# Optimization experiments

Hardware: AMD Instinct MI355X
Metric: run time of the kernel (lower is better)

The kernel has to match this reference:

```python
import jax, jax.numpy as jnp
import numpy as np

B, N, D = 4, 16384, 128       # batch, tokens (mesh points), input_dim
H, DH = 8, 64                 # heads, dim_head
INNER = H * DH


def setup_inputs() -> dict:
    key = jax.random.key(0)
    ks = jax.random.split(key, 7)
    s = 0.02  # weight init scale
    return {
        "queries": jax.random.normal(ks[0], (B, N, D), jnp.float32),
        "keys":    jax.random.normal(ks[1], (B, N, D), jnp.float32),
        "values":  jax.random.normal(ks[2], (B, N, D), jnp.float32),
        "Wq": jax.random.normal(ks[3], (INNER, D), jnp.float32) * s,
        "Wk": jax.random.normal(ks[4], (INNER, D), jnp.float32) * s,
        "Wo": jax.random.normal(ks[5], (D, INNER), jnp.float32) * s,
        "bo": jnp.zeros((D,), jnp.float32),
    }


def _split_heads(x, b, n):
    # [b, n, h*d] -> [b, h, n, d]
    return x.reshape(b, n, H, DH).transpose(0, 2, 1, 3)


def reference(queries, keys, values, Wq, Wk, Wo, bo):
    b, n, _ = queries.shape
    q = _split_heads(queries @ Wq.T, b, n)
    k = _split_heads(keys    @ Wk.T, b, n)
    # NOTE: original source applies to_k to values (bug kept for faithfulness)
    v = _split_heads(values  @ Wk.T, b, n)
    # Galerkin linear attention, associative order: q @ (k^T v) / n.
    # (In the runnable no-mask path the instance norms are computed but
    #  discarded by the original code, so they are omitted here.)
    dots = jnp.einsum('bhnd,bhne->bhde', k, v)          # [b,h,d,d]
    out = jnp.einsum('bhnd,bhde->bhne', q, dots) / n    # [b,h,n,d]
    out = out.transpose(0, 2, 1, 3).reshape(b, n, INNER)
    return out @ Wo.T + bo
```

## Files before the change

kernel.cpp:

```cpp
#include <hip/hip_runtime.h>
#include <hip/hip_bf16.h>

#define BB    4
#define NN    16384
#define DD    128
#define HH    8
#define DHH   64
#define INNER 512
#define PC    64

typedef __attribute__((ext_vector_type(8))) short bf16x8;
typedef __attribute__((ext_vector_type(4))) short short4_t;
typedef __attribute__((ext_vector_type(4))) float f32x4;
typedef unsigned short ushort_t;

#define MFMA(a, b, c) __builtin_amdgcn_mfma_f32_16x16x32_bf16((a), (b), (c), 0, 0, 0)

__device__ __forceinline__ short f2bf(float x) {
    union { float f; unsigned u; } v; v.f = x;
    unsigned u = v.u;
    u += 0x7fffu + ((u >> 16) & 1u);
    return (short)(u >> 16);
}

__device__ __forceinline__ float bf2f(ushort_t us) {
    union { unsigned u; float f; } v;
    v.u = ((unsigned)us) << 16;
    return v.f;
}

__device__ __forceinline__ bf16x8 load_row8(const float* __restrict__ p) {
    f32x4 a = *(const f32x4*)p;
    f32x4 b = *(const f32x4*)(p + 4);
    bf16x8 r;
    r[0] = f2bf(a[0]); r[1] = f2bf(a[1]); r[2] = f2bf(a[2]); r[3] = f2bf(a[3]);
    r[4] = f2bf(b[0]); r[5] = f2bf(b[1]); r[6] = f2bf(b[2]); r[7] = f2bf(b[3]);
    return r;
}

__device__ __forceinline__ bf16x8 load_col8(const float* __restrict__ p, int stride) {
    bf16x8 r;
#pragma unroll
    for (int j = 0; j < 8; ++j) r[j] = f2bf(p[(size_t)j * stride]);
    return r;
}

__global__ __launch_bounds__(512) void k1_partialS_ab(
        const float* __restrict__ keys, const float* __restrict__ vals,
        const float* __restrict__ Wq, const float* __restrict__ Wk,
        const float* __restrict__ Wo,
        ushort_t* __restrict__ partial, ushort_t* __restrict__ Abf,
        ushort_t* __restrict__ BTbf) {
    const int lane = threadIdx.x & 63;
    const int w    = threadIdx.x >> 6;
    const int ml   = lane & 15;
    const int quad = lane >> 4;

    __shared__ short tK[2][32][132];
    __shared__ short tV[2][32][132];

    if (blockIdx.x < BB * PC) {
        const int b     = blockIdx.x >> 6;
        const int chunk = blockIdx.x & (PC - 1);
        const int r0    = chunk * (NN / PC);
        const int mw    = w & 3;
        const int nw    = w >> 2;

        const float* kbase = keys + (size_t)b * NN * DD;
        const float* vbase = vals + (size_t)b * NN * DD;

        const int lin0 = (int)threadIdx.x;
        const int ca0  = (2 * mw + 0) * 16 + ml;
        const int ca1  = (2 * mw + 1) * 16 + ml;

        f32x4 acc[2][4];
#pragma unroll
        for (int i = 0; i < 2; ++i)
#pragma unroll
            for (int t = 0; t < 4; ++t) acc[i][t] = (f32x4){0.f, 0.f, 0.f, 0.f};

        {
            const float* kp = kbase + (size_t)r0 * DD;
            const float* vp = vbase + (size_t)r0 * DD;
#pragma unroll
            for (int it = 0; it < 2; ++it) {
                const int lin = lin0 + it * 512;
                const int row = lin >> 5;
                const int c4  = (lin & 31) << 2;
                f32x4 kk = *(const f32x4*)(kp + (size_t)row * DD + c4);
                f32x4 vv = *(const f32x4*)(vp + (size_t)row * DD + c4);
                short4_t ks, vs;
#pragma unroll
                for (int j = 0; j < 4; ++j) { ks[j] = f2bf(kk[j]); vs[j] = f2bf(vv[j]); }
                *(short4_t*)&tK[0][row][c4] = ks;
                *(short4_t*)&tV[0][row][c4] = vs;
            }
        }
        __syncthreads();

        for (int s = 0; s < 8; ++s) {
            const int cur  = s & 1;
            const bool more = (s < 7);

            f32x4 kreg[2], vreg[2];
            if (more) {
                const float* kp = kbase + (size_t)(r0 + (s + 1) * 32) * DD;
                const float* vp = vbase + (size_t)(r0 + (s + 1) * 32) * DD;
#pragma unroll
                for (int it = 0; it < 2; ++it) {
                    const int lin = lin0 + it * 512;
                    const int row = lin >> 5;
                    const int c4  = (lin & 31) << 2;
                    kreg[it] = *(const f32x4*)(kp + (size_t)row * DD + c4);
                    vreg[it] = *(const f32x4*)(vp + (size_t)row * DD + c4);
                }
            }

            {
                bf16x8 a0, a1;
#pragma unroll
                for (int j = 0; j < 8; ++j) {
                    a0[j] = tK[cur][quad * 8 + j][ca0];
                    a1[j] = tK[cur][quad * 8 + j][ca1];
                }
#pragma unroll
                for (int t = 0; t < 4; ++t) {
                    const int cb = (nw * 4 + t) * 16 + ml;
                    bf16x8 bf;
#pragma unroll
                    for (int j = 0; j < 8; ++j) bf[j] = tV[cur][quad * 8 + j][cb];
                    acc[0][t] = MFMA(a0, bf, acc[0][t]);
                    acc[1][t] = MFMA(a1, bf, acc[1][t]);
                }
            }

            if (more) {
                __syncthreads();
                const int nb = cur ^ 1;
#pragma unroll
                for (int it = 0; it < 2; ++it) {
                    const int lin = lin0 + it * 512;
                    const int row = lin >> 5;
                    const int c4  = (lin & 31) << 2;
                    short4_t ks, vs;
#pragma unroll
                    for (int j = 0; j < 4; ++j) {
                        ks[j] = f2bf(kreg[it][j]);
                        vs[j] = f2bf(vreg[it][j]);
                    }
                    *(short4_t*)&tK[nb][row][c4] = ks;
                    *(short4_t*)&tV[nb][row][c4] = vs;
                }
                __syncthreads();
            }
        }

        ushort_t* outp = partial + (size_t)blockIdx.x * DD * DD;
#pragma unroll
        for (int i = 0; i < 2; ++i) {
            const int mrow = (2 * mw + i) * 16 + quad * 4;
#pragma unroll
            for (int t = 0; t < 4; ++t) {
                const int col = (nw * 4 + t) * 16 + ml;
#pragma unroll
                for (int r = 0; r < 4; ++r)
                    outp[(size_t)(mrow + r) * DD + col] = (ushort_t)f2bf(acc[i][t][r]);
            }
        }
    } else {
        const int ab    = blockIdx.x - BB * PC;
        const int h     = ab & 7;
        const int which = ab >> 3;
        const float* Wkh = Wk + (size_t)h * DHH * DD;

        f32x4 acc[8];
#pragma unroll
        for (int t = 0; t < 8; ++t) acc[t] = (f32x4){0.f, 0.f, 0.f, 0.f};

        if (which == 0) {
            const float* Wqh = Wq + (size_t)h * DHH * DD;
#pragma unroll
            for (int kc = 0; kc < 2; ++kc) {
                const int d0 = kc * 32 + quad * 8;
                bf16x8 a = load_col8(Wqh + (size_t)d0 * DD + w * 16 + ml, DD);
#pragma unroll
                for (int t = 0; t < 8; ++t) {
                    bf16x8 bf = load_col8(Wkh + (size_t)d0 * DD + t * 16 + ml, DD);
                    acc[t] = MFMA(a, bf, acc[t]);
                }
            }
            ushort_t* dst = Abf + (size_t)h * DD * DD;
#pragma unroll
            for (int t = 0; t < 8; ++t)
#pragma unroll
                for (int r = 0; r < 4; ++r)
                    dst[(size_t)(w * 16 + quad * 4 + r) * DD + t * 16 + ml] =
                        (ushort_t)f2bf(acc[t][r]);
        } else {
#pragma unroll
            for (int kc = 0; kc < 2; ++kc) {
                const int e0 = kc * 32 + quad * 8;
                bf16x8 a = load_row8(Wo + (size_t)(w * 16 + ml) * INNER + h * DHH + e0);
#pragma unroll
                for (int t = 0; t < 8; ++t) {
                    bf16x8 bf = load_col8(Wkh + (size_t)e0 * DD + t * 16 + ml, DD);
                    acc[t] = MFMA(a, bf, acc[t]);
                }
            }
            ushort_t* dst = BTbf + (size_t)h * DD * DD;
#pragma unroll
            for (int t = 0; t < 8; ++t)
#pragma unroll
                for (int r = 0; r < 4; ++r)
                    dst[(size_t)(w * 16 + quad * 4 + r) * DD + t * 16 + ml] =
                        (ushort_t)f2bf(acc[t][r]);
        }
    }
}

__global__ __launch_bounds__(256) void k2_reduce(
        const ushort_t* __restrict__ partial, float* __restrict__ S,
        float* __restrict__ G) {
    const int t   = blockIdx.x * 256 + threadIdx.x;
    const int b   = t >> 14;
    const int idx = t & 16383;
    const ushort_t* p = partial + ((size_t)b * PC) * DD * DD + idx;
    float s = 0.f;
#pragma unroll 16
    for (int c = 0; c < PC; ++c) s += bf2f(p[(size_t)c * DD * DD]);
    S[t] = s;
    G[t] = 0.f;
}

__global__ __launch_bounds__(256) void k3_middle(
        const float* __restrict__ S, const ushort_t* __restrict__ Abf,
        const ushort_t* __restrict__ BTbf, float* __restrict__ G) {
    const int b    = blockIdx.x >> 3;
    const int h    = blockIdx.x & 7;
    const int lane = threadIdx.x & 63;
    const int w    = threadIdx.x >> 6;
    const int ml   = lane & 15;
    const int quad = lane >> 4;

    __shared__ short T[128 * 136];

    const float*    Sb = S    + (size_t)b * DD * DD;
    const ushort_t* Ah = Abf  + (size_t)h * DD * DD;
    const ushort_t* Bh = BTbf + (size_t)h * DD * DD;

    {
        f32x4 acc[2][8];
#pragma unroll
        for (int i = 0; i < 2; ++i)
#pragma unroll
            for (int t = 0; t < 8; ++t) acc[i][t] = (f32x4){0.f, 0.f, 0.f, 0.f};
#pragma unroll
        for (int kc = 0; kc < 4; ++kc) {
            const int c0 = kc * 32 + quad * 8;
            bf16x8 a[2];
#pragma unroll
            for (int i = 0; i < 2; ++i)
                a[i] = *(const bf16x8*)&Ah[(size_t)((2 * w + i) * 16 + ml) * DD + c0];
#pragma unroll
            for (int t = 0; t < 8; ++t) {
                bf16x8 bf = load_col8(Sb + (size_t)c0 * DD + t * 16 + ml, DD);
                acc[0][t] = MFMA(a[0], bf, acc[0][t]);
                acc[1][t] = MFMA(a[1], bf, acc[1][t]);
            }
        }
#pragma unroll
        for (int i = 0; i < 2; ++i)
#pragma unroll
            for (int t = 0; t < 8; ++t)
#pragma unroll
                for (int r = 0; r < 4; ++r)
                    T[((2 * w + i) * 16 + quad * 4 + r) * 136 + t * 16 + ml] =
                        f2bf(acc[i][t][r]);
    }
    __syncthreads();

    {
        f32x4 acc[2][8];
#pragma unroll
        for (int i = 0; i < 2; ++i)
#pragma unroll
            for (int t = 0; t < 8; ++t) acc[i][t] = (f32x4){0.f, 0.f, 0.f, 0.f};
#pragma unroll
        for (int kc = 0; kc < 4; ++kc) {
            const int k0 = kc * 32 + quad * 8;
            bf16x8 a[2];
#pragma unroll
            for (int i = 0; i < 2; ++i)
                a[i] = *(const bf16x8*)&T[((2 * w + i) * 16 + ml) * 136 + k0];
#pragma unroll
            for (int t = 0; t < 8; ++t) {
                bf16x8 bf = *(const bf16x8*)&Bh[(size_t)(t * 16 + ml) * DD + k0];
                acc[0][t] = MFMA(a[0], bf, acc[0][t]);
                acc[1][t] = MFMA(a[1], bf, acc[1][t]);
            }
        }
        float* Gb = G + (size_t)b * DD * DD;
#pragma unroll
        for (int i = 0; i < 2; ++i)
#pragma unroll
            for (int t = 0; t < 8; ++t)
#pragma unroll
                for (int r = 0; r < 4; ++r)
                    atomicAdd(&Gb[((2 * w + i) * 16 + quad * 4 + r) * DD + t * 16 + ml],
                              acc[i][t][r]);
    }
}

__global__ __launch_bounds__(512) void k4_final(
        const float* __restrict__ queries, const float* __restrict__ G,
        const float* __restrict__ bo, float* __restrict__ outp) {
    const int b  = blockIdx.x >> 6;
    const int r0 = (blockIdx.x & 63) * 256;

    __shared__ short Gt[128 * 136];
    {
        const float* Gb = G + (size_t)b * DD * DD;
        const float invN = 6.103515625e-05f;
#pragma unroll 4
        for (int it = 0; it < 32; ++it) {
            const int idx = threadIdx.x + it * 512;
            const int cp = idx >> 7, c = idx & 127;
            Gt[c * 136 + cp] = f2bf(Gb[idx] * invN);
        }
    }
    __syncthreads();

    const int lane = threadIdx.x & 63;
    const int w    = threadIdx.x >> 6;
    const int ml   = lane & 15;
    const int quad = lane >> 4;
    const float* qbase = queries + ((size_t)b * NN + r0) * DD;

    f32x4 acc[2][8];
#pragma unroll
    for (int i = 0; i < 2; ++i)
#pragma unroll
        for (int t = 0; t < 8; ++t) acc[i][t] = (f32x4){0.f, 0.f, 0.f, 0.f};

#pragma unroll
    for (int kc = 0; kc < 4; ++kc) {
        const int k0 = kc * 32 + quad * 8;
        bf16x8 a[2];
#pragma unroll
        for (int i = 0; i < 2; ++i)
            a[i] = load_row8(qbase + (size_t)((2 * w + i) * 16 + ml) * DD + k0);
#pragma unroll
        for (int t = 0; t < 8; ++t) {
            bf16x8 bf = *(const bf16x8*)&Gt[(t * 16 + ml) * 136 + k0];
            acc[0][t] = MFMA(a[0], bf, acc[0][t]);
            acc[1][t] = MFMA(a[1], bf, acc[1][t]);
        }
    }

    float* ob = outp + ((size_t)b * NN + r0) * DD;
#pragma unroll
    for (int t = 0; t < 8; ++t) {
        const int c = t * 16 + ml;
        const float boc = bo[c];
#pragma unroll
        for (int i = 0; i < 2; ++i)
#pragma unroll
            for (int r = 0; r < 4; ++r)
                ob[(size_t)((2 * w + i) * 16 + quad * 4 + r) * DD + c] =
                    acc[i][t][r] + boc;
    }
}

extern "C" void kernel_launch(void* const* d_in, const int* in_sizes, int n_in,
                              void* d_out, int out_size, void* d_ws, size_t ws_size,
                              hipStream_t stream) {
    const float* queries = (const float*)d_in[0];
    const float* keys    = (const float*)d_in[1];
    const float* values  = (const float*)d_in[2];
    const float* Wq      = (const float*)d_in[3];
    const float* Wk      = (const float*)d_in[4];
    const float* Wo      = (const float*)d_in[5];
    const float* bo      = (const float*)d_in[6];
    float* out = (float*)d_out;

    float* S = (float*)d_ws;
    float* G = S + (size_t)BB * DD * DD;
    ushort_t* Abf     = (ushort_t*)(G + (size_t)BB * DD * DD);
    ushort_t* BTbf    = Abf  + (size_t)HH * DD * DD;
    ushort_t* partial = BTbf + (size_t)HH * DD * DD;

    hipLaunchKernelGGL(k1_partialS_ab, dim3(BB * PC + 16), dim3(512), 0, stream,
                       keys, values, Wq, Wk, Wo, partial, Abf, BTbf);
    hipLaunchKernelGGL(k2_reduce, dim3(256), dim3(256), 0, stream,
                       partial, S, G);
    hipLaunchKernelGGL(k3_middle, dim3(BB * HH), dim3(256), 0, stream,
                       S, Abf, BTbf, G);
    hipLaunchKernelGGL(k4_final, dim3(256), dim3(512), 0, stream,
                       queries, G, bo, out);
}
```

Baseline: 171.9 us.

## Fuse four Galerkin attention kernels into one cooperative kernel with grid syncs

Merges the partial-S, reduce, middle-product and final-output kernels into a single cooperative launch of 256 blocks, with grid.sync between phases and shared memory reused across them. The aim is to remove the launch overhead and inter-kernel gaps between four small launches. In exchange, the tiny middle phases now run on a few blocks while the rest wait at grid barriers, and the k3 work is spread over 8 waves of 512 threads instead of 4. The cooperative launch requires all 256 blocks to be co-resident.

```diff
diff --git a/kernel.cpp b/kernel.cpp
--- a/kernel.cpp
+++ b/kernel.cpp
@@ -1,5 +1,6 @@
 #include <hip/hip_runtime.h>
 #include <hip/hip_bf16.h>
+#include <hip/hip_cooperative_groups.h>
 
 #define BB    4
 #define NN    16384
@@ -45,21 +46,28 @@
     return r;
 }
 
-__global__ __launch_bounds__(512) void k1_partialS_ab(
-        const float* __restrict__ keys, const float* __restrict__ vals,
-        const float* __restrict__ Wq, const float* __restrict__ Wk,
-        const float* __restrict__ Wo,
-        ushort_t* __restrict__ partial, ushort_t* __restrict__ Abf,
-        ushort_t* __restrict__ BTbf) {
+__global__ __launch_bounds__(512) void fused_galerkin(
+        const float* __restrict__ queries, const float* __restrict__ keys,
+        const float* __restrict__ vals,   const float* __restrict__ Wq,
+        const float* __restrict__ Wk,     const float* __restrict__ Wo,
+        const float* __restrict__ bo,     float* __restrict__ outp,
+        float* __restrict__ S,            float* __restrict__ G,
+        ushort_t* __restrict__ Abf,       ushort_t* __restrict__ BTbf,
+        ushort_t* __restrict__ partial) {
+    namespace cg = cooperative_groups;
+    cg::grid_group grid = cg::this_grid();
+
+    __shared__ __align__(16) short smem[17408];
+
     const int lane = threadIdx.x & 63;
     const int w    = threadIdx.x >> 6;
     const int ml   = lane & 15;
     const int quad = lane >> 4;
 
-    __shared__ short tK[2][32][132];
-    __shared__ short tV[2][32][132];
-
-    if (blockIdx.x < BB * PC) {
+    {
+        short* tK = smem;
+        short* tV = smem + 8448;
+
         const int b     = blockIdx.x >> 6;
         const int chunk = blockIdx.x & (PC - 1);
         const int r0    = chunk * (NN / PC);
@@ -92,14 +100,14 @@
                 short4_t ks, vs;
 #pragma unroll
                 for (int j = 0; j < 4; ++j) { ks[j] = f2bf(kk[j]); vs[j] = f2bf(vv[j]); }
-                *(short4_t*)&tK[0][row][c4] = ks;
-                *(short4_t*)&tV[0][row][c4] = vs;
+                *(short4_t*)&tK[(0 * 32 + row) * 132 + c4] = ks;
+                *(short4_t*)&tV[(0 * 32 + row) * 132 + c4] = vs;
             }
         }
         __syncthreads();
 
         for (int s = 0; s < 8; ++s) {
-            const int cur  = s & 1;
+            const int cur   = s & 1;
             const bool more = (s < 7);
 
             f32x4 kreg[2], vreg[2];
@@ -120,15 +128,16 @@
                 bf16x8 a0, a1;
 #pragma unroll
                 for (int j = 0; j < 8; ++j) {
-                    a0[j] = tK[cur][quad * 8 + j][ca0];
-                    a1[j] = tK[cur][quad * 8 + j][ca1];
+                    a0[j] = tK[(cur * 32 + quad * 8 + j) * 132 + ca0];
+                    a1[j] = tK[(cur * 32 + quad * 8 + j) * 132 + ca1];
                 }
 #pragma unroll
                 for (int t = 0; t < 4; ++t) {
                     const int cb = (nw * 4 + t) * 16 + ml;
                     bf16x8 bf;
 #pragma unroll
-                    for (int j = 0; j < 8; ++j) bf[j] = tV[cur][quad * 8 + j][cb];
+                    for (int j = 0; j < 8; ++j)
+                        bf[j] = tV[(cur * 32 + quad * 8 + j) * 132 + cb];
                     acc[0][t] = MFMA(a0, bf, acc[0][t]);
                     acc[1][t] = MFMA(a1, bf, acc[1][t]);
                 }
@@ -148,14 +157,14 @@
                         ks[j] = f2bf(kreg[it][j]);
                         vs[j] = f2bf(vreg[it][j]);
                     }
-                    *(short4_t*)&tK[nb][row][c4] = ks;
-                    *(short4_t*)&tV[nb][row][c4] = vs;
+                    *(short4_t*)&tK[(nb * 32 + row) * 132 + c4] = ks;
+                    *(short4_t*)&tV[(nb * 32 + row) * 132 + c4] = vs;
                 }
                 __syncthreads();
             }
         }
 
-        ushort_t* outp = partial + (size_t)blockIdx.x * DD * DD;
+        ushort_t* outpart = partial + (size_t)blockIdx.x * DD * DD;
 #pragma unroll
         for (int i = 0; i < 2; ++i) {
             const int mrow = (2 * mw + i) * 16 + quad * 4;
@@ -164,11 +173,25 @@
                 const int col = (nw * 4 + t) * 16 + ml;
 #pragma unroll
                 for (int r = 0; r < 4; ++r)
-                    outp[(size_t)(mrow + r) * DD + col] = (ushort_t)f2bf(acc[i][t][r]);
-            }
-        }
-    } else {
-        const int ab    = blockIdx.x - BB * PC;
+                    outpart[(size_t)(mrow + r) * DD + col] = (ushort_t)f2bf(acc[i][t][r]);
+            }
+        }
+    }
+
+    grid.sync();
+
+    if (blockIdx.x < 128) {
+        const int gid = (int)blockIdx.x * 512 + (int)threadIdx.x;
+        const int b   = gid >> 14;
+        const int idx = gid & 16383;
+        const ushort_t* p = partial + ((size_t)b * PC) * DD * DD + idx;
+        float s = 0.f;
+#pragma unroll 16
+        for (int c = 0; c < PC; ++c) s += bf2f(p[(size_t)c * DD * DD]);
+        S[gid] = s;
+        G[gid] = 0.f;
+    } else if (blockIdx.x < 144) {
+        const int ab    = blockIdx.x - 128;
         const int h     = ab & 7;
         const int which = ab >> 3;
         const float* Wkh = Wk + (size_t)h * DHH * DD;
@@ -216,158 +239,118 @@
                         (ushort_t)f2bf(acc[t][r]);
         }
     }
-}
-
-__global__ __launch_bounds__(256) void k2_reduce(
-        const ushort_t* __restrict__ partial, float* __restrict__ S,
-        float* __restrict__ G) {
-    const int t   = blockIdx.x * 256 + threadIdx.x;
-    const int b   = t >> 14;
-    const int idx = t & 16383;
-    const ushort_t* p = partial + ((size_t)b * PC) * DD * DD + idx;
-    float s = 0.f;
-#pragma unroll 16
-    for (int c = 0; c < PC; ++c) s += bf2f(p[(size_t)c * DD * DD]);
-    S[t] = s;
-    G[t] = 0.f;
-}
-
-__global__ __launch_bounds__(256) void k3_middle(
-        const float* __restrict__ S, const ushort_t* __restrict__ Abf,
-        const ushort_t* __restrict__ BTbf, float* __restrict__ G) {
-    const int b    = blockIdx.x >> 3;
-    const int h    = blockIdx.x & 7;
-    const int lane = threadIdx.x & 63;
-    const int w    = threadIdx.x >> 6;
-    const int ml   = lane & 15;
-    const int quad = lane >> 4;
-
-    __shared__ short T[128 * 136];
-
-    const float*    Sb = S    + (size_t)b * DD * DD;
-    const ushort_t* Ah = Abf  + (size_t)h * DD * DD;
-    const ushort_t* Bh = BTbf + (size_t)h * DD * DD;
+
+    grid.sync();
+
+    if (blockIdx.x < BB * HH) {
+        const int b = blockIdx.x >> 3;
+        const int h = blockIdx.x & 7;
+        short* T = smem;
+
+        const float*    Sb = S    + (size_t)b * DD * DD;
+        const ushort_t* Ah = Abf  + (size_t)h * DD * DD;
+        const ushort_t* Bh = BTbf + (size_t)h * DD * DD;
+
+        {
+            f32x4 acc[8];
+#pragma unroll
+            for (int t = 0; t < 8; ++t) acc[t] = (f32x4){0.f, 0.f, 0.f, 0.f};
+#pragma unroll
+            for (int kc = 0; kc < 4; ++kc) {
+                const int c0 = kc * 32 + quad * 8;
+                bf16x8 a = *(const bf16x8*)&Ah[(size_t)(w * 16 + ml) * DD + c0];
+#pragma unroll
+                for (int t = 0; t < 8; ++t) {
+                    bf16x8 bf = load_col8(Sb + (size_t)c0 * DD + t * 16 + ml, DD);
+                    acc[t] = MFMA(a, bf, acc[t]);
+                }
+            }
+#pragma unroll
+            for (int t = 0; t < 8; ++t)
+#pragma unroll
+                for (int r = 0; r < 4; ++r)
+                    T[(w * 16 + quad * 4 + r) * 136 + t * 16 + ml] = f2bf(acc[t][r]);
+        }
+        __syncthreads();
+
+        {
+            f32x4 acc[8];
+#pragma unroll
+            for (int t = 0; t < 8; ++t) acc[t] = (f32x4){0.f, 0.f, 0.f, 0.f};
+#pragma unroll
+            for (int kc = 0; kc < 4; ++kc) {
+                const int k0 = kc * 32 + quad * 8;
+                bf16x8 a = *(const bf16x8*)&T[(w * 16 + ml) * 136 + k0];
+#pragma unroll
+                for (int t = 0; t < 8; ++t) {
+                    bf16x8 bf = *(const bf16x8*)&Bh[(size_t)(t * 16 + ml) * DD + k0];
+                    acc[t] = MFMA(a, bf, acc[t]);
+                }
+            }
+            float* Gb = G + (size_t)b * DD * DD;
+#pragma unroll
+            for (int t = 0; t < 8; ++t)
+#pragma unroll
+                for (int r = 0; r < 4; ++r)
+                    atomicAdd(&Gb[(w * 16 + quad * 4 + r) * DD + t * 16 + ml],
+                              acc[t][r]);
+        }
+    }
+
+    grid.sync();
 
     {
+        short* Gt = smem;
+        const int b  = blockIdx.x >> 6;
+        const int r0 = (blockIdx.x & 63) * 256;
+
+        {
+            const float* Gb = G + (size_t)b * DD * DD;
+            const float invN = 6.103515625e-05f;
+#pragma unroll 4
+            for (int it = 0; it < 32; ++it) {
+                const int idx = (int)threadIdx.x + it * 512;
+                const int cp = idx >> 7, c = idx & 127;
+                Gt[c * 136 + cp] = f2bf(Gb[idx] * invN);
+            }
+        }
+        __syncthreads();
+
+        const float* qbase = queries + ((size_t)b * NN + r0) * DD;
+
         f32x4 acc[2][8];
 #pragma unroll
         for (int i = 0; i < 2; ++i)
 #pragma unroll
             for (int t = 0; t < 8; ++t) acc[i][t] = (f32x4){0.f, 0.f, 0.f, 0.f};
-#pragma unroll
-        for (int kc = 0; kc < 4; ++kc) {
-            const int c0 = kc * 32 + quad * 8;
-            bf16x8 a[2];
-#pragma unroll
-            for (int i = 0; i < 2; ++i)
-                a[i] = *(const bf16x8*)&Ah[(size_t)((2 * w + i) * 16 + ml) * DD + c0];
-#pragma unroll
-            for (int t = 0; t < 8; ++t) {
-                bf16x8 bf = load_col8(Sb + (size_t)c0 * DD + t * 16 + ml, DD);
-                acc[0][t] = MFMA(a[0], bf, acc[0][t]);
-                acc[1][t] = MFMA(a[1], bf, acc[1][t]);
-            }
-        }
-#pragma unroll
-        for (int i = 0; i < 2; ++i)
-#pragma unroll
-            for (int t = 0; t < 8; ++t)
-#pragma unroll
-                for (int r = 0; r < 4; ++r)
-                    T[((2 * w + i) * 16 + quad * 4 + r) * 136 + t * 16 + ml] =
-                        f2bf(acc[i][t][r]);
-    }
-    __syncthreads();
-
-    {
-        f32x4 acc[2][8];
-#pragma unroll
-        for (int i = 0; i < 2; ++i)
-#pragma unroll
-            for (int t = 0; t < 8; ++t) acc[i][t] = (f32x4){0.f, 0.f, 0.f, 0.f};
+
 #pragma unroll
         for (int kc = 0; kc < 4; ++kc) {
             const int k0 = kc * 32 + quad * 8;
             bf16x8 a[2];
 #pragma unroll
             for (int i = 0; i < 2; ++i)
-                a[i] = *(const bf16x8*)&T[((2 * w + i) * 16 + ml) * 136 + k0];
+                a[i] = load_row8(qbase + (size_t)((2 * w + i) * 16 + ml) * DD + k0);
 #pragma unroll
             for (int t = 0; t < 8; ++t) {
-                bf16x8 bf = *(const bf16x8*)&Bh[(size_t)(t * 16 + ml) * DD + k0];
+                bf16x8 bf = *(const bf16x8*)&Gt[(t * 16 + ml) * 136 + k0];
                 acc[0][t] = MFMA(a[0], bf, acc[0][t]);
                 acc[1][t] = MFMA(a[1], bf, acc[1][t]);
             }
         }
-        float* Gb = G + (size_t)b * DD * DD;
-#pragma unroll
-        for (int i = 0; i < 2; ++i)
-#pragma unroll
-            for (int t = 0; t < 8; ++t)
-#pragma unroll
-                for (int r = 0; r < 4; ++r)
-                    atomicAdd(&Gb[((2 * w + i) * 16 + quad * 4 + r) * DD + t * 16 + ml],
-                              acc[i][t][r]);
-    }
-}
-
-__global__ __launch_bounds__(512) void k4_final(
-        const float* __restrict__ queries, const float* __restrict__ G,
-        const float* __restrict__ bo, float* __restrict__ outp) {
-    const int b  = blockIdx.x >> 6;
-    const int r0 = (blockIdx.x & 63) * 256;
-
-    __shared__ short Gt[128 * 136];
-    {
-        const float* Gb = G + (size_t)b * DD * DD;
-        const float invN = 6.103515625e-05f;
-#pragma unroll 4
-        for (int it = 0; it < 32; ++it) {
-            const int idx = threadIdx.x + it * 512;
-            const int cp = idx >> 7, c = idx & 127;
-            Gt[c * 136 + cp] = f2bf(Gb[idx] * invN);
-        }
-    }
-    __syncthreads();
-
-    const int lane = threadIdx.x & 63;
-    const int w    = threadIdx.x >> 6;
-    const int ml   = lane & 15;
-    const int quad = lane >> 4;
-    const float* qbase = queries + ((size_t)b * NN + r0) * DD;
-
-    f32x4 acc[2][8];
-#pragma unroll
-    for (int i = 0; i < 2; ++i)
-#pragma unroll
-        for (int t = 0; t < 8; ++t) acc[i][t] = (f32x4){0.f, 0.f, 0.f, 0.f};
-
-#pragma unroll
-    for (int kc = 0; kc < 4; ++kc) {
-        const int k0 = kc * 32 + quad * 8;
-        bf16x8 a[2];
-#pragma unroll
-        for (int i = 0; i < 2; ++i)
-            a[i] = load_row8(qbase + (size_t)((2 * w + i) * 16 + ml) * DD + k0);
+
+        float* ob = outp + ((size_t)b * NN + r0) * DD;
 #pragma unroll
         for (int t = 0; t < 8; ++t) {
-            bf16x8 bf = *(const bf16x8*)&Gt[(t * 16 + ml) * 136 + k0];
-            acc[0][t] = MFMA(a[0], bf, acc[0][t]);
-            acc[1][t] = MFMA(a[1], bf, acc[1][t]);
-        }
-    }
-
-    float* ob = outp + ((size_t)b * NN + r0) * DD;
-#pragma unroll
-    for (int t = 0; t < 8; ++t) {
-        const int c = t * 16 + ml;
-        const float boc = bo[c];
-#pragma unroll
-        for (int i = 0; i < 2; ++i)
-#pragma unroll
-            for (int r = 0; r < 4; ++r)
-                ob[(size_t)((2 * w + i) * 16 + quad * 4 + r) * DD + c] =
-                    acc[i][t][r] + boc;
+            const int c = t * 16 + ml;
+            const float boc = bo[c];
+#pragma unroll
+            for (int i = 0; i < 2; ++i)
+#pragma unroll
+                for (int r = 0; r < 4; ++r)
+                    ob[(size_t)((2 * w + i) * 16 + quad * 4 + r) * DD + c] =
+                        acc[i][t][r] + boc;
+        }
     }
 }
 
@@ -389,12 +372,11 @@
     ushort_t* BTbf    = Abf  + (size_t)HH * DD * DD;
     ushort_t* partial = BTbf + (size_t)HH * DD * DD;
 
-    hipLaunchKernelGGL(k1_partialS_ab, dim3(BB * PC + 16), dim3(512), 0, stream,
-                       keys, values, Wq, Wk, Wo, partial, Abf, BTbf);
-    hipLaunchKernelGGL(k2_reduce, dim3(256), dim3(256), 0, stream,
-                       partial, S, G);
-    hipLaunchKernelGGL(k3_middle, dim3(BB * HH), dim3(256), 0, stream,
-                       S, Abf, BTbf, G);
-    hipLaunchKernelGGL(k4_final, dim3(256), dim3(512), 0, stream,
-                       queries, G, bo, out);
-}
+    void* args[] = {
+        (void*)&queries, (void*)&keys, (void*)&values, (void*)&Wq,
+        (void*)&Wk, (void*)&Wo, (void*)&bo, (void*)&out,
+        (void*)&S, (void*)&G, (void*)&Abf, (void*)&BTbf, (void*)&partial
+    };
+    hipLaunchCooperativeKernel((const void*)fused_galerkin, dim3(256), dim3(512),
+                               args, 0, stream);
+}
```

Result: slower. 278.1 us (+61.8%).

## Double grid parallelism in partial-S and final kernels, stage S in LDS

Applied to the files above, without the earlier changes.

Doubles the number of key/value chunks so the partial-S kernel launches twice as many blocks, each covering half the rows, and halves rows per block in the final kernel to double its grid. k3 now uses 512 threads, one 16-row tile per wave, and transposes S into LDS as bf16 instead of strided global column loads. k2 reads two bf16 partials per 32-bit load. More partials mean more reduction traffic in k2 and a larger workspace footprint, in exchange for better occupancy on the large kernels.

```diff
diff --git a/kernel.cpp b/kernel.cpp
--- a/kernel.cpp
+++ b/kernel.cpp
@@ -7,7 +7,7 @@
 #define HH    8
 #define DHH   64
 #define INNER 512
-#define PC    64
+#define PC    128
 
 typedef __attribute__((ext_vector_type(8))) short bf16x8;
 typedef __attribute__((ext_vector_type(4))) short short4_t;
@@ -45,7 +45,7 @@
     return r;
 }
 
-__global__ __launch_bounds__(512) void k1_partialS_ab(
+__global__ __launch_bounds__(512, 4) void k1_partialS_ab(
         const float* __restrict__ keys, const float* __restrict__ vals,
         const float* __restrict__ Wq, const float* __restrict__ Wk,
         const float* __restrict__ Wo,
@@ -60,7 +60,7 @@
     __shared__ short tV[2][32][132];
 
     if (blockIdx.x < BB * PC) {
-        const int b     = blockIdx.x >> 6;
+        const int b     = blockIdx.x >> 7;
         const int chunk = blockIdx.x & (PC - 1);
         const int r0    = chunk * (NN / PC);
         const int mw    = w & 3;
@@ -98,9 +98,9 @@
         }
         __syncthreads();
 
-        for (int s = 0; s < 8; ++s) {
-            const int cur  = s & 1;
-            const bool more = (s < 7);
+        for (int s = 0; s < 4; ++s) {
+            const int cur   = s & 1;
+            const bool more = (s < 3);
 
             f32x4 kreg[2], vreg[2];
             if (more) {
@@ -221,18 +221,24 @@
 __global__ __launch_bounds__(256) void k2_reduce(
         const ushort_t* __restrict__ partial, float* __restrict__ S,
         float* __restrict__ G) {
-    const int t   = blockIdx.x * 256 + threadIdx.x;
-    const int b   = t >> 14;
-    const int idx = t & 16383;
-    const ushort_t* p = partial + ((size_t)b * PC) * DD * DD + idx;
-    float s = 0.f;
+    const int tid = blockIdx.x * 256 + threadIdx.x;
+    const int e   = tid * 2;
+    const int b   = e >> 14;
+    const int idx = e & 16383;
+    const unsigned* p32 =
+        (const unsigned*)(partial + ((size_t)b * PC) * DD * DD + idx);
+    float s0 = 0.f, s1 = 0.f;
 #pragma unroll 16
-    for (int c = 0; c < PC; ++c) s += bf2f(p[(size_t)c * DD * DD]);
-    S[t] = s;
-    G[t] = 0.f;
-}
-
-__global__ __launch_bounds__(256) void k3_middle(
+    for (int c = 0; c < PC; ++c) {
+        const unsigned u = p32[(size_t)c * (DD * DD / 2)];
+        s0 += bf2f((ushort_t)(u & 0xffffu));
+        s1 += bf2f((ushort_t)(u >> 16));
+    }
+    S[e] = s0;  S[e + 1] = s1;
+    G[e] = 0.f; G[e + 1] = 0.f;
+}
+
+__global__ __launch_bounds__(512) void k3_middle(
         const float* __restrict__ S, const ushort_t* __restrict__ Abf,
         const ushort_t* __restrict__ BTbf, float* __restrict__ G) {
     const int b    = blockIdx.x >> 3;
@@ -242,80 +248,75 @@
     const int ml   = lane & 15;
     const int quad = lane >> 4;
 
-    __shared__ short T[128 * 136];
+    __shared__ short ST[128 * 136];
+    __shared__ short T [128 * 136];
 
     const float*    Sb = S    + (size_t)b * DD * DD;
     const ushort_t* Ah = Abf  + (size_t)h * DD * DD;
     const ushort_t* Bh = BTbf + (size_t)h * DD * DD;
 
+#pragma unroll
+    for (int it = 0; it < 8; ++it) {
+        const int idx4 = ((int)threadIdx.x + it * 512) * 4;
+        const int c  = idx4 >> 7;
+        const int cp = idx4 & 127;
+        f32x4 v = *(const f32x4*)(Sb + idx4);
+#pragma unroll
+        for (int j = 0; j < 4; ++j) ST[(cp + j) * 136 + c] = f2bf(v[j]);
+    }
+    __syncthreads();
+
     {
-        f32x4 acc[2][8];
-#pragma unroll
-        for (int i = 0; i < 2; ++i)
-#pragma unroll
-            for (int t = 0; t < 8; ++t) acc[i][t] = (f32x4){0.f, 0.f, 0.f, 0.f};
+        f32x4 acc[8];
+#pragma unroll
+        for (int t = 0; t < 8; ++t) acc[t] = (f32x4){0.f, 0.f, 0.f, 0.f};
 #pragma unroll
         for (int kc = 0; kc < 4; ++kc) {
             const int c0 = kc * 32 + quad * 8;
-            bf16x8 a[2];
-#pragma unroll
-            for (int i = 0; i < 2; ++i)
-                a[i] = *(const bf16x8*)&Ah[(size_t)((2 * w + i) * 16 + ml) * DD + c0];
+            bf16x8 a = *(const bf16x8*)&Ah[(size_t)(w * 16 + ml) * DD + c0];
 #pragma unroll
             for (int t = 0; t < 8; ++t) {
-                bf16x8 bf = load_col8(Sb + (size_t)c0 * DD + t * 16 + ml, DD);
-                acc[0][t] = MFMA(a[0], bf, acc[0][t]);
-                acc[1][t] = MFMA(a[1], bf, acc[1][t]);
-            }
-        }
-#pragma unroll
-        for (int i = 0; i < 2; ++i)
-#pragma unroll
-            for (int t = 0; t < 8; ++t)
-#pragma unroll
-                for (int r = 0; r < 4; ++r)
-                    T[((2 * w + i) * 16 + quad * 4 + r) * 136 + t * 16 + ml] =
-                        f2bf(acc[i][t][r]);
+                bf16x8 bf = *(const bf16x8*)&ST[(t * 16 + ml) * 136 + c0];
+                acc[t] = MFMA(a, bf, acc[t]);
+            }
+        }
+#pragma unroll
+        for (int t = 0; t < 8; ++t)
+#pragma unroll
+            for (int r = 0; r < 4; ++r)
+                T[(w * 16 + quad * 4 + r) * 136 + t * 16 + ml] = f2bf(acc[t][r]);
     }
     __syncthreads();
 
     {
-        f32x4 acc[2][8];
-#pragma unroll
-        for (int i = 0; i < 2; ++i)
-#pragma unroll
-            for (int t = 0; t < 8; ++t) acc[i][t] = (f32x4){0.f, 0.f, 0.f, 0.f};
+        f32x4 acc[8];
+#pragma unroll
+        for (int t = 0; t < 8; ++t) acc[t] = (f32x4){0.f, 0.f, 0.f, 0.f};
 #pragma unroll
         for (int kc = 0; kc < 4; ++kc) {
             const int k0 = kc * 32 + quad * 8;
-            bf16x8 a[2];
-#pragma unroll
-            for (int i = 0; i < 2; ++i)
-                a[i] = *(const bf16x8*)&T[((2 * w + i) * 16 + ml) * 136 + k0];
+            bf16x8 a = *(const bf16x8*)&T[(w * 16 + ml) * 136 + k0];
 #pragma unroll
             for (int t = 0; t < 8; ++t) {
                 bf16x8 bf = *(const bf16x8*)&Bh[(size_t)(t * 16 + ml) * DD + k0];
-                acc[0][t] = MFMA(a[0], bf, acc[0][t]);
-                acc[1][t] = MFMA(a[1], bf, acc[1][t]);
+                acc[t] = MFMA(a, bf, acc[t]);
             }
         }
         float* Gb = G + (size_t)b * DD * DD;
 #pragma unroll
-        for (int i = 0; i < 2; ++i)
-#pragma unroll
-            for (int t = 0; t < 8; ++t)
-#pragma unroll
-                for (int r = 0; r < 4; ++r)
-                    atomicAdd(&Gb[((2 * w + i) * 16 + quad * 4 + r) * DD + t * 16 + ml],
-                              acc[i][t][r]);
-    }
-}
-
-__global__ __launch_bounds__(512) void k4_final(
+        for (int t = 0; t < 8; ++t)
+#pragma unroll
+            for (int r = 0; r < 4; ++r)
+                atomicAdd(&Gb[(w * 16 + quad * 4 + r) * DD + t * 16 + ml],
+                          acc[t][r]);
+    }
+}
+
+__global__ __launch_bounds__(512, 4) void k4_final(
         const float* __restrict__ queries, const float* __restrict__ G,
         const float* __restrict__ bo, float* __restrict__ outp) {
-    const int b  = blockIdx.x >> 6;
-    const int r0 = (blockIdx.x & 63) * 256;
+    const int b  = blockIdx.x >> 7;
+    const int r0 = (blockIdx.x & 127) * 128;
 
     __shared__ short Gt[128 * 136];
     {
@@ -323,7 +324,7 @@
         const float invN = 6.103515625e-05f;
 #pragma unroll 4
         for (int it = 0; it < 32; ++it) {
-            const int idx = threadIdx.x + it * 512;
+            const int idx = (int)threadIdx.x + it * 512;
             const int cp = idx >> 7, c = idx & 127;
             Gt[c * 136 + cp] = f2bf(Gb[idx] * invN);
         }
@@ -336,24 +337,18 @@
     const int quad = lane >> 4;
     const float* qbase = queries + ((size_t)b * NN + r0) * DD;
 
-    f32x4 acc[2][8];
-#pragma unroll
-    for (int i = 0; i < 2; ++i)
-#pragma unroll
-        for (int t = 0; t < 8; ++t) acc[i][t] = (f32x4){0.f, 0.f, 0.f, 0.f};
+    f32x4 acc[8];
+#pragma unroll
+    for (int t = 0; t < 8; ++t) acc[t] = (f32x4){0.f, 0.f, 0.f, 0.f};
 
 #pragma unroll
     for (int kc = 0; kc < 4; ++kc) {
         const int k0 = kc * 32 + quad * 8;
-        bf16x8 a[2];
-#pragma unroll
-        for (int i = 0; i < 2; ++i)
-            a[i] = load_row8(qbase + (size_t)((2 * w + i) * 16 + ml) * DD + k0);
+        bf16x8 a = load_row8(qbase + (size_t)(w * 16 + ml) * DD + k0);
 #pragma unroll
         for (int t = 0; t < 8; ++t) {
             bf16x8 bf = *(const bf16x8*)&Gt[(t * 16 + ml) * 136 + k0];
-            acc[0][t] = MFMA(a[0], bf, acc[0][t]);
-            acc[1][t] = MFMA(a[1], bf, acc[1][t]);
+            acc[t] = MFMA(a, bf, acc[t]);
         }
     }
 
@@ -363,11 +358,8 @@
         const int c = t * 16 + ml;
         const float boc = bo[c];
 #pragma unroll
-        for (int i = 0; i < 2; ++i)
-#pragma unroll
-            for (int r = 0; r < 4; ++r)
-                ob[(size_t)((2 * w + i) * 16 + quad * 4 + r) * DD + c] =
-                    acc[i][t][r] + boc;
+        for (int r = 0; r < 4; ++r)
+            ob[(size_t)(w * 16 + quad * 4 + r) * DD + c] = acc[t][r] + boc;
     }
 }
 
@@ -391,10 +383,10 @@
 
     hipLaunchKernelGGL(k1_partialS_ab, dim3(BB * PC + 16), dim3(512), 0, stream,
                        keys, values, Wq, Wk, Wo, partial, Abf, BTbf);
-    hipLaunchKernelGGL(k2_reduce, dim3(256), dim3(256), 0, stream,
+    hipLaunchKernelGGL(k2_reduce, dim3(128), dim3(256), 0, stream,
                        partial, S, G);
-    hipLaunchKernelGGL(k3_middle, dim3(BB * HH), dim3(256), 0, stream,
+    hipLaunchKernelGGL(k3_middle, dim3(BB * HH), dim3(512), 0, stream,
                        S, Abf, BTbf, G);
-    hipLaunchKernelGGL(k4_final, dim3(256), dim3(512), 0, stream,
+    hipLaunchKernelGGL(k4_final, dim3(512), dim3(512), 0, stream,
                        queries, G, bo, out);
 }
```

Result: no change. 169.9 us (-1.2%).
